# Kernel tuning notes

Measured on AMD Instinct MI355X. Metric: run time of the kernel, lower is better.

## Reference

```python
import jax, jax.numpy as jnp
import numpy as np

# Hard-coded dims from the module
D, L, R, H, M, T = 64, 90, 5760, 1024, 1024, 20
N_OUT = 3
B = 64  # per-timestep batch; feature has B*T rows


def setup_inputs() -> dict:
    key = jax.random.key(0)
    ks = jax.random.split(key, 20)
    def w(i, shape, fan_in):
        return jax.random.normal(ks[i], shape, dtype=jnp.float32) * (1.0 / np.sqrt(fan_in))
    return {
        "feature": jax.random.normal(ks[0], (B * T, L, D), dtype=jnp.float32),
        # additive attention params (alpha over L locations)
        "attn_Wx": w(1, (D, D), D),
        "attn_Wh": w(2, (H, D), H),
        "attn_v": w(3, (D,), D),
        # LSTM (PyTorch gate order i,f,g,o)
        "W_ih": w(4, (4 * H, R), R),
        "W_hh": w(5, (4 * H, H), H),
        "b_ih": jnp.zeros((4 * H,), jnp.float32),
        "b_hh": jnp.zeros((4 * H,), jnp.float32),
        # output head
        "Wh_w": w(6, (M, H), H),
        "Wh_b": jnp.zeros((M,), jnp.float32),
        "Wy_w": w(7, (M, R), R),
        "Wu_w": w(8, (N_OUT, M), M),
        "Wu_b": jnp.zeros((N_OUT,), jnp.float32),
        # LSTM-state initializers
        "iWh_w": w(9, (H, D), D),
        "iWh_b": jnp.zeros((H,), jnp.float32),
        "iWc_w": w(10, (H, D), D),
        "iWc_b": jnp.zeros((H,), jnp.float32),
    }


def reference(feature, attn_Wx, attn_Wh, attn_v, W_ih, W_hh, b_ih, b_hh,
              Wh_w, Wh_b, Wy_w, Wu_w, Wu_b, iWh_w, iWh_b, iWc_w, iWc_b):
    batch = feature.shape[0] // T
    seq = feature.reshape(batch, T, L, D).transpose(1, 0, 2, 3)  # [T,B,L,D]

    # initializeLSTM (no_grad in the original -> stop_gradient)
    f0 = jnp.mean(seq[0], axis=1)                                  # [B,D]
    h0 = jax.lax.stop_gradient(jnp.tanh(f0 @ iWh_w.T + iWh_b))     # [B,H]
    c0 = jax.lax.stop_gradient(jnp.tanh(f0 @ iWc_w.T + iWc_b))     # [B,H]

    def step(carry, xt):  # xt: [B,L,D]
        h, c = carry
        # additive attention over L locations
        e = jnp.tanh(jnp.einsum('bld,da->bla', xt, attn_Wx)
                     + (h @ attn_Wh)[:, None, :]) @ attn_v          # [B,L]
        alpha = jax.nn.softmax(e, axis=1)
        visual = (xt * alpha[:, :, None]).reshape(-1, R)            # [B,R]
        # single LSTM step (PyTorch gate order i,f,g,o)
        gates = visual @ W_ih.T + b_ih + h @ W_hh.T + b_hh          # [B,4H]
        i, f, g, o = jnp.split(gates, 4, axis=-1)
        c = jax.nn.sigmoid(f) * c + jax.nn.sigmoid(i) * jnp.tanh(g)
        h = jax.nn.sigmoid(o) * jnp.tanh(c)
        # ut = Wu(Wh(h) + Wy(visual)); dropout omitted for determinism
        ut = (h @ Wh_w.T + Wh_b + visual @ Wy_w.T) @ Wu_w.T + Wu_b  # [B,n_out]
        return (h, c), ut

    _, outs = jax.lax.scan(step, (h0, c0), seq)                     # [T,B,n_out]
    return outs.transpose(1, 0, 2).reshape(batch * T, -1)
```

## Files before the change

### kernel.cpp

```cpp
#include <hip/hip_runtime.h>
#include <math.h>

typedef _Float16 half8 __attribute__((ext_vector_type(8)));
typedef _Float16 half4v __attribute__((ext_vector_type(4)));
typedef _Float16 half2v __attribute__((ext_vector_type(2)));
typedef float floatx16 __attribute__((ext_vector_type(16)));

#define TT 20
#define NB 64
#define LL 90
#define DD 64
#define RR 5760
#define HH 1024
#define NG 4096
#define KT 6784
#define CH0 90
#define CHT 106

__device__ __forceinline__ float sigm(float x) { return 1.f / (1.f + expf(-x)); }

__global__ __launch_bounds__(256) void k_conv2(const float* __restrict__ s1, _Float16* __restrict__ d1, int n1,
                                               const float* __restrict__ s2, _Float16* __restrict__ d2, int n2) {
    int i = (blockIdx.x * 256 + threadIdx.x) * 4;
    const float* s; _Float16* d;
    if (i < n1) { s = s1 + i; d = d1 + i; }
    else if ((i -= n1) < n2) { s = s2 + i; d = d2 + i; }
    else return;
    const float4 v = *(const float4*)s;
    half4v o;
    o[0] = (_Float16)v.x; o[1] = (_Float16)v.y;
    o[2] = (_Float16)v.z; o[3] = (_Float16)v.w;
    *(half4v*)d = o;
}

__global__ __launch_bounds__(256) void k_whT(const float* __restrict__ Wh, _Float16* __restrict__ WhT) {
    const int idx = blockIdx.x * 256 + threadIdx.x;
    const int a = idx >> 8, k4 = (idx & 255) * 4;
    half4v o;
#pragma unroll
    for (int u = 0; u < 4; ++u) o[u] = (_Float16)Wh[(size_t)(k4 + u) * DD + a];
    *(half4v*)(WhT + (size_t)a * HH + k4) = o;
}

__global__ __launch_bounds__(256) void k_xproj(const float* __restrict__ feat,
                                               const float* __restrict__ Wx,
                                               _Float16* __restrict__ xp) {
    __shared__ float sWx[DD * DD];
    __shared__ float sx[16 * DD];
    const int row = blockIdx.x;
    const int tid = threadIdx.x;
    for (int e = tid * 4; e < DD * DD; e += 1024)
        *(float4*)(sWx + e) = *(const float4*)(Wx + e);
    const int a4 = tid & 15, lg = tid >> 4;
    const float* frow = feat + (size_t)row * RR;
    for (int lb = 0; lb < LL; lb += 16) {
        __syncthreads();
        { int e = tid * 4; int ls = e >> 6, dd = e & 63;
          if (lb + ls < LL) *(float4*)(sx + e) = *(const float4*)(frow + (lb + ls) * DD + dd); }
        __syncthreads();
        const int l = lb + lg;
        if (l < LL) {
            float a0 = 0, a1 = 0, a2 = 0, a3 = 0;
            for (int dd = 0; dd < DD; ++dd) {
                const float xv = sx[lg * DD + dd];
                const float4 wv = *(const float4*)(sWx + dd * DD + a4 * 4);
                a0 += xv * wv.x; a1 += xv * wv.y; a2 += xv * wv.z; a3 += xv * wv.w;
            }
            half4v o;
            o[0] = (_Float16)a0; o[1] = (_Float16)a1; o[2] = (_Float16)a2; o[3] = (_Float16)a3;
            *(half4v*)(xp + (size_t)row * RR + l * DD + a4 * 4) = o;
        }
    }
}

__global__ __launch_bounds__(256) void k_init(const float* __restrict__ feat,
        const float* __restrict__ iWh_w, const float* __restrict__ iWh_b,
        const float* __restrict__ iWc_w, const float* __restrict__ iWc_b,
        float* __restrict__ h, float* __restrict__ c, _Float16* __restrict__ h16) {
    __shared__ float f0p[4][DD];
    __shared__ float f0[DD];
    const int b = blockIdx.x, tid = threadIdx.x;
    const int dd = tid & 63, lg = tid >> 6;
    const float* frow = feat + (size_t)(b * TT) * RR;
    float p = 0;
    for (int l = lg; l < LL; l += 4) p += frow[l * DD + dd];
    f0p[lg][dd] = p;
    __syncthreads();
    if (tid < DD) f0[tid] = (f0p[0][tid] + f0p[1][tid] + f0p[2][tid] + f0p[3][tid]) * (1.0f / LL);
    __syncthreads();
    for (int o = tid; o < HH; o += 256) {
        float ah = iWh_b[o], ac = iWc_b[o];
        for (int d0 = 0; d0 < DD; d0 += 4) {
            const float4 wh = *(const float4*)(iWh_w + (size_t)o * DD + d0);
            const float4 wc = *(const float4*)(iWc_w + (size_t)o * DD + d0);
            ah += f0[d0] * wh.x + f0[d0 + 1] * wh.y + f0[d0 + 2] * wh.z + f0[d0 + 3] * wh.w;
            ac += f0[d0] * wc.x + f0[d0 + 1] * wc.y + f0[d0 + 2] * wc.z + f0[d0 + 3] * wc.w;
        }
        const float hv = tanhf(ah), cv = tanhf(ac);
        h[b * HH + o] = hv; c[b * HH + o] = cv;
        h16[b * HH + o] = (_Float16)hv;
    }
}

__global__ __launch_bounds__(512) void k_step(int tattn, int do_cell,
        const float* __restrict__ gpart, const float* __restrict__ b_ih,
        const float* __restrict__ b_hh, const float* __restrict__ cin,
        float* __restrict__ cout, _Float16* __restrict__ h16,
        _Float16* __restrict__ H16, const float* __restrict__ h0buf,
        const float* __restrict__ feat, const _Float16* __restrict__ xp,
        const _Float16* __restrict__ WhT, const float* __restrict__ v,
        _Float16* __restrict__ V16) {
    __shared__ float sh[HH];
    __shared__ float hWhp[8][DD];
    __shared__ float hWh[DD];
    __shared__ float sv[DD];
    __shared__ float ep[LL][4];
    __shared__ float se[128];
    __shared__ float red[128];
    __shared__ float salpha[LL];
    const int b = blockIdx.x, qv = blockIdx.y, tid = threadIdx.x;
    const int t = tattn;
    if (tid < DD) sv[tid] = v[tid];

    if (do_cell) {
        const int j0 = tid * 2;
        float ag[4][2];
#pragma unroll
        for (int g = 0; g < 4; ++g) { ag[g][0] = 0.f; ag[g][1] = 0.f; }
#pragma unroll
        for (int sp = 0; sp < 8; ++sp) {
            const float* P = gpart + ((size_t)sp * NB + b) * NG;
#pragma unroll
            for (int g = 0; g < 4; ++g) {
                const float2 pv = *(const float2*)(P + g * HH + j0);
                ag[g][0] += pv.x; ag[g][1] += pv.y;
            }
        }
#pragma unroll
        for (int g = 0; g < 4; ++g) {
            const float2 bi = *(const float2*)(b_ih + g * HH + j0);
            const float2 bh = *(const float2*)(b_hh + g * HH + j0);
            ag[g][0] += bi.x + bh.x; ag[g][1] += bi.y + bh.y;
        }
        const float2 cold = *(const float2*)(cin + (size_t)b * HH + j0);
        float co[2] = { cold.x, cold.y };
        float2 cnew; half2v hh2;
#pragma unroll
        for (int q = 0; q < 2; ++q) {
            const float cv = sigm(ag[1][q]) * co[q] + sigm(ag[0][q]) * tanhf(ag[2][q]);
            const float hv = sigm(ag[3][q]) * tanhf(cv);
            ((float*)&cnew)[q] = cv;
            hh2[q] = (_Float16)hv;
            sh[j0 + q] = hv;
        }
        *(float2*)(cout + (size_t)b * HH + j0) = cnew;
        *(half2v*)(h16 + (size_t)b * HH + j0) = hh2;
        *(half2v*)(H16 + ((size_t)(t - 1) * NB + b) * HH + j0) = hh2;
    } else {
        for (int e = tid; e < HH; e += 512) sh[e] = h0buf[(size_t)b * HH + e];
    }
    __syncthreads();
    if (t >= TT) return;

    { const int a = tid & 63, q8 = tid >> 6;
      const _Float16* Wq = WhT + (size_t)a * HH + q8 * 128;
      const float* shq = sh + q8 * 128;
      float p = 0.f;
#pragma unroll
      for (int k = 0; k < 128; k += 8) {
          const half8 wv = *(const half8*)(Wq + k);
#pragma unroll
          for (int u = 0; u < 8; ++u) p += shq[k + u] * (float)wv[u];
      }
      hWhp[q8][a] = p; }
    __syncthreads();
    if (tid < DD) {
        float s = 0.f;
#pragma unroll
        for (int q = 0; q < 8; ++q) s += hWhp[q][tid];
        hWh[tid] = s;
    }
    __syncthreads();

    const size_t frow = (size_t)(b * TT + t) * RR;
    if (tid < 360) {
        const int l = tid >> 2, qq = tid & 3;
        const _Float16* xr = xp + frow + l * DD + qq * 16;
        const half8 x0 = *(const half8*)(xr);
        const half8 x1 = *(const half8*)(xr + 8);
        float acc = 0.f;
#pragma unroll
        for (int i = 0; i < 8; ++i)
            acc += tanhf((float)x0[i] + hWh[qq * 16 + i]) * sv[qq * 16 + i];
#pragma unroll
        for (int i = 0; i < 8; ++i)
            acc += tanhf((float)x1[i] + hWh[qq * 16 + 8 + i]) * sv[qq * 16 + 8 + i];
        ep[l][qq] = acc;
    }
    __syncthreads();
    if (tid < LL) se[tid] = ep[tid][0] + ep[tid][1] + ep[tid][2] + ep[tid][3];
    else if (tid < 128) se[tid] = -1e30f;
    __syncthreads();
    if (tid < 128) red[tid] = se[tid];
    __syncthreads();
    for (int s = 64; s; s >>= 1) { if (tid < s) red[tid] = fmaxf(red[tid], red[tid + s]); __syncthreads(); }
    const float mx = red[0];
    __syncthreads();
    float ex = 0.f;
    if (tid < LL) { ex = expf(se[tid] - mx); salpha[tid] = ex; }
    if (tid < 128) red[tid] = ex;
    __syncthreads();
    for (int s = 64; s; s >>= 1) { if (tid < s) red[tid] += red[tid + s]; __syncthreads(); }
    const float inv = 1.f / red[0];
    __syncthreads();
    if (tid < LL) salpha[tid] *= inv;
    __syncthreads();

    _Float16* vout = V16 + ((size_t)t * NB + b) * RR;
    const float* fr = feat + frow;
    const int ebeg = qv * 1440;
    const int e = ebeg + tid * 4;
    if (e < ebeg + 1440) {
        const float4 u4 = *(const float4*)(fr + e);
        const float al = salpha[e >> 6];
        half4v o;
        o[0] = (_Float16)(u4.x * al); o[1] = (_Float16)(u4.y * al);
        o[2] = (_Float16)(u4.z * al); o[3] = (_Float16)(u4.w * al);
        *(half4v*)(vout + e) = o;
    }
}

__device__ __forceinline__ void stage_tile(const char* src, size_t stride, char* lds, int ln) {
    const char* g = src + (size_t)(ln >> 3) * stride + (((ln & 7) ^ (ln >> 3)) << 4);
#pragma unroll
    for (int i = 0; i < 8; ++i)
        __builtin_amdgcn_global_load_lds(
            (const __attribute__((address_space(1))) void*)(g + (size_t)(i * 8) * stride),
            (__attribute__((address_space(3))) void*)(lds + i * 1024), 16, 0, 0);
}

struct Src2 { const char* p0; size_t s0; const char* p1; size_t s1; };

__device__ __forceinline__ const char* chunk_ptr(const Src2& s, int c, size_t& stride) {
    if (c < CH0) { stride = s.s0; return s.p0 + (size_t)c * 128; }
    stride = s.s1; return s.p1 + (size_t)(c - CH0) * 128;
}

__global__ __launch_bounds__(128) void k_gates(int t, const _Float16* __restrict__ V16,
        const _Float16* __restrict__ h16, const _Float16* __restrict__ Wih,
        const _Float16* __restrict__ Whh, float* __restrict__ gpart) {
    __shared__ char smem[65536];
    const int bid = blockIdx.x;
    const int kb = bid >> 6;
    const int nt = ((bid & 7) << 3) | ((bid >> 3) & 7);
    const int tid = threadIdx.x, w = tid >> 6, ln = tid & 63;
    char* wlds = smem + w * 32768;

    const _Float16* Vt = V16 + (size_t)t * NB * RR;
    Src2 As = { (const char*)Vt, (size_t)RR * 2, (const char*)h16, (size_t)HH * 2 };
    Src2 Bs = { (const char*)(Wih + (size_t)(nt * 64) * RR), (size_t)RR * 2,
                (const char*)(Whh + (size_t)(nt * 64) * HH), (size_t)HH * 2 };

    floatx16 acc00, acc01, acc10, acc11;
#pragma unroll
    for (int i = 0; i < 16; ++i) { acc00[i] = 0.f; acc01[i] = 0.f; acc10[i] = 0.f; acc11[i] = 0.f; }

    const int start = kb * 2 + w;
    const int r = ln & 31;
    const int xsw = (r & 7) << 4;
    const int fo = (ln >> 5) * 16;
    const int rbyte = r * 128;

    int c = start, bsel = 0;
    { size_t st; const char* p = chunk_ptr(As, c, st); stage_tile(p, st, wlds, ln);
      p = chunk_ptr(Bs, c, st); stage_tile(p, st, wlds + 8192, ln); }
    while (true) {
        const int cn = c + 16;
        if (cn < CHT) {
            char* nl = wlds + ((bsel ^ 1) << 14);
            size_t st; const char* p = chunk_ptr(As, cn, st); stage_tile(p, st, nl, ln);
            p = chunk_ptr(Bs, cn, st); stage_tile(p, st, nl + 8192, ln);
            asm volatile("s_waitcnt vmcnt(16)" ::: "memory");
        } else {
            asm volatile("s_waitcnt vmcnt(0)" ::: "memory");
        }
        __builtin_amdgcn_sched_barrier(0);
        const char* LA = wlds + (bsel << 14);
        const char* LB = LA + 8192;
#pragma unroll
        for (int kk = 0; kk < 4; ++kk) {
            const int o = ((kk * 32 + fo) ^ xsw);
            const half8 a0 = *(const half8*)(LA + rbyte + o);
            const half8 a1 = *(const half8*)(LA + 4096 + rbyte + o);
            const half8 b0 = *(const half8*)(LB + rbyte + o);
            const half8 b1 = *(const half8*)(LB + 4096 + rbyte + o);
            acc00 = __builtin_amdgcn_mfma_f32_32x32x16_f16(a0, b0, acc00, 0, 0, 0);
            acc01 = __builtin_amdgcn_mfma_f32_32x32x16_f16(a0, b1, acc01, 0, 0, 0);
            acc10 = __builtin_amdgcn_mfma_f32_32x32x16_f16(a1, b0, acc10, 0, 0, 0);
            acc11 = __builtin_amdgcn_mfma_f32_32x32x16_f16(a1, b1, acc11, 0, 0, 0);
        }
        if (cn >= CHT) break;
        c = cn; bsel ^= 1;
    }
    __syncthreads();
    float* Rg = (float*)(smem + w * 16384);
    const int rbase = 4 * (ln >> 5), lr = ln & 31;
#pragma unroll
    for (int q = 0; q < 16; ++q) {
        const int row = rbase + (q & 3) + 8 * (q >> 2);
        Rg[row * 64 + lr]             = acc00[q];
        Rg[row * 64 + 32 + lr]        = acc01[q];
        Rg[(row + 32) * 64 + lr]      = acc10[q];
        Rg[(row + 32) * 64 + 32 + lr] = acc11[q];
    }
    __syncthreads();
    const float* R0 = (const float*)smem;
    const float* R1 = (const float*)(smem + 16384);
    float* Cout = gpart + (size_t)kb * (NB * NG);
    for (int e = tid * 4; e < 4096; e += 512) {
        const float4 u = *(const float4*)(R0 + e);
        const float4 v2 = *(const float4*)(R1 + e);
        float4 s2; s2.x = u.x + v2.x; s2.y = u.y + v2.y; s2.z = u.z + v2.z; s2.w = u.w + v2.w;
        const int row = e >> 6, col = e & 63;
        *(float4*)(Cout + (size_t)row * NG + nt * 64 + col) = s2;
    }
}

__global__ __launch_bounds__(256) void k_wfuse(const float* __restrict__ Wy,
        const float* __restrict__ Whw, const float* __restrict__ Wu,
        const float* __restrict__ Whb, const float* __restrict__ Wub,
        _Float16* __restrict__ Wyu16, float* __restrict__ cst) {
    __shared__ float sWu[3 * HH];
    __shared__ float part[4][3][64];
    const int tid = threadIdx.x;
    for (int e = tid * 4; e < 3 * HH; e += 1024)
        *(float4*)(sWu + e) = *(const float4*)(Wu + e);
    __syncthreads();
    if (blockIdx.x == CHT) {
        float a0 = 0, a1 = 0, a2 = 0;
        for (int m = tid; m < HH; m += 256) {
            const float wb = Whb[m];
            a0 += sWu[m] * wb; a1 += sWu[HH + m] * wb; a2 += sWu[2 * HH + m] * wb;
        }
        __shared__ float rp[3][256];
        rp[0][tid] = a0; rp[1][tid] = a1; rp[2][tid] = a2;
        __syncthreads();
        for (int s = 128; s; s >>= 1) {
            if (tid < s) { rp[0][tid] += rp[0][tid + s]; rp[1][tid] += rp[1][tid + s]; rp[2][tid] += rp[2][tid + s]; }
            __syncthreads();
        }
        if (tid < 3) cst[tid] = rp[tid][0] + Wub[tid];
        return;
    }
    const int kk = tid & 63, qm = tid >> 6;
    const int k = blockIdx.x * 64 + kk;
    const float* src; size_t ld;
    if (blockIdx.x < CH0) { src = Wy + k; ld = RR; }
    else { src = Whw + (k - RR); ld = HH; }
    float a0 = 0, a1 = 0, a2 = 0;
    for (int m = qm * 256; m < qm * 256 + 256; ++m) {
        const float val = src[(size_t)m * ld];
        a0 += sWu[m] * val; a1 += sWu[HH + m] * val; a2 += sWu[2 * HH + m] * val;
    }
    part[qm][0][kk] = a0; part[qm][1][kk] = a1; part[qm][2][kk] = a2;
    __syncthreads();
    if (tid < 192) {
        const int j = tid >> 6, k2 = tid & 63;
        const float s = part[0][j][k2] + part[1][j][k2] + part[2][j][k2] + part[3][j][k2];
        Wyu16[(size_t)j * KT + blockIdx.x * 64 + k2] = (_Float16)s;
    }
}

__global__ __launch_bounds__(256) void k_final2(const _Float16* __restrict__ V16,
        const _Float16* __restrict__ H16, const _Float16* __restrict__ Wyu,
        const float* __restrict__ cst, float* __restrict__ out) {
    __shared__ float rp[4][3];
    const int r = blockIdx.x, tid = threadIdx.x;
    const _Float16* vrow = V16 + (size_t)r * RR;
    const _Float16* hrow = H16 + (size_t)r * HH;
    float a0 = 0, a1 = 0, a2 = 0;
    for (int e = tid * 8; e < KT; e += 2048) {
        half8 x;
        if (e < RR) x = *(const half8*)(vrow + e);
        else        x = *(const half8*)(hrow + (e - RR));
        const half8 w0 = *(const half8*)(Wyu + e);
        const half8 w1 = *(const half8*)(Wyu + KT + e);
        const half8 w2 = *(const half8*)(Wyu + 2 * KT + e);
#pragma unroll
        for (int i = 0; i < 8; ++i) {
            const float xv = (float)x[i];
            a0 += xv * (float)w0[i]; a1 += xv * (float)w1[i]; a2 += xv * (float)w2[i];
        }
    }
    for (int o = 32; o > 0; o >>= 1) {
        a0 += __shfl_down(a0, o, 64); a1 += __shfl_down(a1, o, 64); a2 += __shfl_down(a2, o, 64);
    }
    const int wv = tid >> 6;
    if ((tid & 63) == 0) { rp[wv][0] = a0; rp[wv][1] = a1; rp[wv][2] = a2; }
    __syncthreads();
    if (tid < 3) {
        const float x = rp[0][tid] + rp[1][tid] + rp[2][tid] + rp[3][tid] + cst[tid];
        const int b = r & 63, ts = r >> 6;
        out[((size_t)b * TT + ts) * 3 + tid] = x;
    }
}

extern "C" void kernel_launch(void* const* d_in, const int* in_sizes, int n_in,
                              void* d_out, int out_size, void* d_ws, size_t ws_size,
                              hipStream_t stream) {
    (void)in_sizes; (void)n_in; (void)out_size;
    const float* feature = (const float*)d_in[0];
    const float* attn_Wx = (const float*)d_in[1];
    const float* attn_Wh = (const float*)d_in[2];
    const float* attn_v  = (const float*)d_in[3];
    const float* W_ih    = (const float*)d_in[4];
    const float* W_hh    = (const float*)d_in[5];
    const float* b_ih    = (const float*)d_in[6];
    const float* b_hh    = (const float*)d_in[7];
    const float* Wh_w    = (const float*)d_in[8];
    const float* Wh_b    = (const float*)d_in[9];
    const float* Wy_w    = (const float*)d_in[10];
    const float* Wu_w    = (const float*)d_in[11];
    const float* Wu_b    = (const float*)d_in[12];
    const float* iWh_w   = (const float*)d_in[13];
    const float* iWh_b   = (const float*)d_in[14];
    const float* iWc_w   = (const float*)d_in[15];
    const float* iWc_b   = (const float*)d_in[16];
    float* out = (float*)d_out;

    char* ws = (char*)d_ws;
    size_t off = 0;
    auto alloc = [&](size_t bytes) { void* p = ws + off; off += (bytes + 255) & ~(size_t)255; return p; };
    _Float16* Wih16 = (_Float16*)alloc((size_t)NG * RR * 2);
    _Float16* Whh16 = (_Float16*)alloc((size_t)NG * HH * 2);
    _Float16* WhT16 = (_Float16*)alloc((size_t)DD * HH * 2);
    _Float16* xp16  = (_Float16*)alloc((size_t)1280 * RR * 2);
    _Float16* V16   = (_Float16*)alloc((size_t)TT * NB * RR * 2);
    _Float16* H16   = (_Float16*)alloc((size_t)TT * NB * HH * 2);
    float*    hbuf  = (float*)alloc((size_t)NB * HH * 4);
    float*    cb0   = (float*)alloc((size_t)NB * HH * 4);
    float*    cb1   = (float*)alloc((size_t)NB * HH * 4);
    _Float16* h16   = (_Float16*)alloc((size_t)NB * HH * 2);
    float*    gpart = (float*)alloc((size_t)8 * NB * NG * 4);
    _Float16* Wyu16 = (_Float16*)alloc((size_t)3 * KT * 2);
    float*    cstb  = (float*)alloc(16);
    if (ws_size < off) return;

    const int nconv = NG * RR + NG * HH;
    k_conv2<<<(nconv / 4 + 255) / 256, 256, 0, stream>>>(W_ih, Wih16, NG * RR,
                                                         W_hh, Whh16, NG * HH);
    k_whT<<<64, 256, 0, stream>>>(attn_Wh, WhT16);
    k_xproj<<<1280, 256, 0, stream>>>(feature, attn_Wx, xp16);
    k_wfuse<<<CHT + 1, 256, 0, stream>>>(Wy_w, Wh_w, Wu_w, Wh_b, Wu_b, Wyu16, cstb);
    k_init<<<64, 256, 0, stream>>>(feature, iWh_w, iWh_b, iWc_w, iWc_b, hbuf, cb0, h16);

    k_step<<<dim3(64, 4), 512, 0, stream>>>(0, 0, gpart, b_ih, b_hh, cb0, cb1,
                                            h16, H16, hbuf, feature, xp16, WhT16,
                                            attn_v, V16);
    for (int t = 0; t < TT; ++t) {
        k_gates<<<512, 128, 0, stream>>>(t, V16, h16, Wih16, Whh16, gpart);
        const float* cin = (t & 1) ? cb1 : cb0;
        float* cou       = (t & 1) ? cb0 : cb1;
        k_step<<<dim3(64, 4), 512, 0, stream>>>(t + 1, 1, gpart, b_ih, b_hh, cin, cou,
                                                h16, H16, hbuf, feature, xp16, WhT16,
                                                attn_v, V16);
    }

    k_final2<<<1280, 256, 0, stream>>>(V16, H16, Wyu16, cstb, out);
}
```

Measured before the change: 649.5 us.

## Fuse attention/cell step and gate GEMM into one producer-consumer kernel

Merges the per-timestep attention/LSTM-cell kernel and the gate GEMM into a single launch. 64 producer blocks compute the cell update, attention and context vector, then signal a per-timestep atomic counter. The 448 consumer blocks first stage their weight tile, then spin on that counter before loading the activation tile. Split-K drops from 8 to 7 and a separate kernel finishes the last cell update. This roughly halves the kernel launches and overlaps weight loading with the producers' work. In exchange, each batch row now uses one 128-thread producer block instead of four 512-thread blocks, and correctness relies on the producers being resident while consumers spin.

Measured after the change: 1.438 ms. +121.4%, slower.

```diff
diff --git a/kernel.cpp b/kernel.cpp
--- a/kernel.cpp
+++ b/kernel.cpp
@@ -3,7 +3,6 @@
 
 typedef _Float16 half8 __attribute__((ext_vector_type(8)));
 typedef _Float16 half4v __attribute__((ext_vector_type(4)));
-typedef _Float16 half2v __attribute__((ext_vector_type(2)));
 typedef float floatx16 __attribute__((ext_vector_type(16)));
 
 #define TT 20
@@ -16,6 +15,10 @@
 #define KT 6784
 #define CH0 90
 #define CHT 106
+#define NPROD 64
+#define SPLITK 7
+#define NCONS 448
+#define KSTRIDE 14
 
 __device__ __forceinline__ float sigm(float x) { return 1.f / (1.f + expf(-x)); }
 
@@ -76,10 +79,12 @@
 __global__ __launch_bounds__(256) void k_init(const float* __restrict__ feat,
         const float* __restrict__ iWh_w, const float* __restrict__ iWh_b,
         const float* __restrict__ iWc_w, const float* __restrict__ iWc_b,
-        float* __restrict__ h, float* __restrict__ c, _Float16* __restrict__ h16) {
+        float* __restrict__ h, float* __restrict__ c, _Float16* __restrict__ h16,
+        int* __restrict__ done) {
     __shared__ float f0p[4][DD];
     __shared__ float f0[DD];
     const int b = blockIdx.x, tid = threadIdx.x;
+    if (b == 0 && tid < 32) done[tid] = 0;
     const int dd = tid & 63, lg = tid >> 6;
     const float* frow = feat + (size_t)(b * TT) * RR;
     float p = 0;
@@ -102,134 +107,6 @@
     }
 }
 
-__global__ __launch_bounds__(512) void k_step(int tattn, int do_cell,
-        const float* __restrict__ gpart, const float* __restrict__ b_ih,
-        const float* __restrict__ b_hh, const float* __restrict__ cin,
-        float* __restrict__ cout, _Float16* __restrict__ h16,
-        _Float16* __restrict__ H16, const float* __restrict__ h0buf,
-        const float* __restrict__ feat, const _Float16* __restrict__ xp,
-        const _Float16* __restrict__ WhT, const float* __restrict__ v,
-        _Float16* __restrict__ V16) {
-    __shared__ float sh[HH];
-    __shared__ float hWhp[8][DD];
-    __shared__ float hWh[DD];
-    __shared__ float sv[DD];
-    __shared__ float ep[LL][4];
-    __shared__ float se[128];
-    __shared__ float red[128];
-    __shared__ float salpha[LL];
-    const int b = blockIdx.x, qv = blockIdx.y, tid = threadIdx.x;
-    const int t = tattn;
-    if (tid < DD) sv[tid] = v[tid];
-
-    if (do_cell) {
-        const int j0 = tid * 2;
-        float ag[4][2];
-#pragma unroll
-        for (int g = 0; g < 4; ++g) { ag[g][0] = 0.f; ag[g][1] = 0.f; }
-#pragma unroll
-        for (int sp = 0; sp < 8; ++sp) {
-            const float* P = gpart + ((size_t)sp * NB + b) * NG;
-#pragma unroll
-            for (int g = 0; g < 4; ++g) {
-                const float2 pv = *(const float2*)(P + g * HH + j0);
-                ag[g][0] += pv.x; ag[g][1] += pv.y;
-            }
-        }
-#pragma unroll
-        for (int g = 0; g < 4; ++g) {
-            const float2 bi = *(const float2*)(b_ih + g * HH + j0);
-            const float2 bh = *(const float2*)(b_hh + g * HH + j0);
-            ag[g][0] += bi.x + bh.x; ag[g][1] += bi.y + bh.y;
-        }
-        const float2 cold = *(const float2*)(cin + (size_t)b * HH + j0);
-        float co[2] = { cold.x, cold.y };
-        float2 cnew; half2v hh2;
-#pragma unroll
-        for (int q = 0; q < 2; ++q) {
-            const float cv = sigm(ag[1][q]) * co[q] + sigm(ag[0][q]) * tanhf(ag[2][q]);
-            const float hv = sigm(ag[3][q]) * tanhf(cv);
-            ((float*)&cnew)[q] = cv;
-            hh2[q] = (_Float16)hv;
-            sh[j0 + q] = hv;
-        }
-        *(float2*)(cout + (size_t)b * HH + j0) = cnew;
-        *(half2v*)(h16 + (size_t)b * HH + j0) = hh2;
-        *(half2v*)(H16 + ((size_t)(t - 1) * NB + b) * HH + j0) = hh2;
-    } else {
-        for (int e = tid; e < HH; e += 512) sh[e] = h0buf[(size_t)b * HH + e];
-    }
-    __syncthreads();
-    if (t >= TT) return;
-
-    { const int a = tid & 63, q8 = tid >> 6;
-      const _Float16* Wq = WhT + (size_t)a * HH + q8 * 128;
-      const float* shq = sh + q8 * 128;
-      float p = 0.f;
-#pragma unroll
-      for (int k = 0; k < 128; k += 8) {
-          const half8 wv = *(const half8*)(Wq + k);
-#pragma unroll
-          for (int u = 0; u < 8; ++u) p += shq[k + u] * (float)wv[u];
-      }
-      hWhp[q8][a] = p; }
-    __syncthreads();
-    if (tid < DD) {
-        float s = 0.f;
-#pragma unroll
-        for (int q = 0; q < 8; ++q) s += hWhp[q][tid];
-        hWh[tid] = s;
-    }
-    __syncthreads();
-
-    const size_t frow = (size_t)(b * TT + t) * RR;
-    if (tid < 360) {
-        const int l = tid >> 2, qq = tid & 3;
-        const _Float16* xr = xp + frow + l * DD + qq * 16;
-        const half8 x0 = *(const half8*)(xr);
-        const half8 x1 = *(const half8*)(xr + 8);
-        float acc = 0.f;
-#pragma unroll
-        for (int i = 0; i < 8; ++i)
-            acc += tanhf((float)x0[i] + hWh[qq * 16 + i]) * sv[qq * 16 + i];
-#pragma unroll
-        for (int i = 0; i < 8; ++i)
-            acc += tanhf((float)x1[i] + hWh[qq * 16 + 8 + i]) * sv[qq * 16 + 8 + i];
-        ep[l][qq] = acc;
-    }
-    __syncthreads();
-    if (tid < LL) se[tid] = ep[tid][0] + ep[tid][1] + ep[tid][2] + ep[tid][3];
-    else if (tid < 128) se[tid] = -1e30f;
-    __syncthreads();
-    if (tid < 128) red[tid] = se[tid];
-    __syncthreads();
-    for (int s = 64; s; s >>= 1) { if (tid < s) red[tid] = fmaxf(red[tid], red[tid + s]); __syncthreads(); }
-    const float mx = red[0];
-    __syncthreads();
-    float ex = 0.f;
-    if (tid < LL) { ex = expf(se[tid] - mx); salpha[tid] = ex; }
-    if (tid < 128) red[tid] = ex;
-    __syncthreads();
-    for (int s = 64; s; s >>= 1) { if (tid < s) red[tid] += red[tid + s]; __syncthreads(); }
-    const float inv = 1.f / red[0];
-    __syncthreads();
-    if (tid < LL) salpha[tid] *= inv;
-    __syncthreads();
-
-    _Float16* vout = V16 + ((size_t)t * NB + b) * RR;
-    const float* fr = feat + frow;
-    const int ebeg = qv * 1440;
-    const int e = ebeg + tid * 4;
-    if (e < ebeg + 1440) {
-        const float4 u4 = *(const float4*)(fr + e);
-        const float al = salpha[e >> 6];
-        half4v o;
-        o[0] = (_Float16)(u4.x * al); o[1] = (_Float16)(u4.y * al);
-        o[2] = (_Float16)(u4.z * al); o[3] = (_Float16)(u4.w * al);
-        *(half4v*)(vout + e) = o;
-    }
-}
-
 __device__ __forceinline__ void stage_tile(const char* src, size_t stride, char* lds, int ln) {
     const char* g = src + (size_t)(ln >> 3) * stride + (((ln & 7) ^ (ln >> 3)) << 4);
 #pragma unroll
@@ -246,14 +123,136 @@
     stride = s.s1; return s.p1 + (size_t)(c - CH0) * 128;
 }
 
-__global__ __launch_bounds__(128) void k_gates(int t, const _Float16* __restrict__ V16,
-        const _Float16* __restrict__ h16, const _Float16* __restrict__ Wih,
-        const _Float16* __restrict__ Whh, float* __restrict__ gpart) {
+__global__ __launch_bounds__(128) void k_sf(int t,
+        const _Float16* __restrict__ Wih, const _Float16* __restrict__ Whh,
+        const _Float16* __restrict__ WhT, const float* __restrict__ v,
+        const float* __restrict__ b_ih, const float* __restrict__ b_hh,
+        const float* __restrict__ hbuf, const float* __restrict__ cin,
+        float* __restrict__ cout, _Float16* __restrict__ h16,
+        _Float16* __restrict__ H16, const float* __restrict__ feat,
+        const _Float16* __restrict__ xp, _Float16* __restrict__ V16,
+        float* __restrict__ gpart, int* __restrict__ done) {
     __shared__ char smem[65536];
-    const int bid = blockIdx.x;
-    const int kb = bid >> 6;
-    const int nt = ((bid & 7) << 3) | ((bid >> 3) & 7);
-    const int tid = threadIdx.x, w = tid >> 6, ln = tid & 63;
+    const int bid = blockIdx.x, tid = threadIdx.x;
+
+    if (bid < NPROD) {
+        const int b = bid;
+        float* sh     = (float*)smem;
+        float* hWhp   = sh + HH;
+        float* hWh    = hWhp + 128;
+        float* sv     = hWh + 64;
+        float* salpha = sv + 64;
+        float* red2   = salpha + 96;
+        if (tid < DD) sv[tid] = v[tid];
+
+        if (t > 0) {
+            const int j0 = tid * 8;
+            float ag[4][8];
+#pragma unroll
+            for (int g = 0; g < 4; ++g)
+#pragma unroll
+                for (int u = 0; u < 8; ++u) ag[g][u] = 0.f;
+            for (int sp = 0; sp < SPLITK; ++sp) {
+                const float* P = gpart + ((size_t)sp * NB + b) * NG;
+#pragma unroll
+                for (int g = 0; g < 4; ++g) {
+                    const float4 p0 = *(const float4*)(P + g * HH + j0);
+                    const float4 p1 = *(const float4*)(P + g * HH + j0 + 4);
+                    ag[g][0] += p0.x; ag[g][1] += p0.y; ag[g][2] += p0.z; ag[g][3] += p0.w;
+                    ag[g][4] += p1.x; ag[g][5] += p1.y; ag[g][6] += p1.z; ag[g][7] += p1.w;
+                }
+            }
+#pragma unroll
+            for (int g = 0; g < 4; ++g) {
+                const float* bi = b_ih + g * HH + j0;
+                const float* bh = b_hh + g * HH + j0;
+#pragma unroll
+                for (int u = 0; u < 8; ++u) ag[g][u] += bi[u] + bh[u];
+            }
+            const float4 ca = *(const float4*)(cin + (size_t)b * HH + j0);
+            const float4 cb4 = *(const float4*)(cin + (size_t)b * HH + j0 + 4);
+            const float co[8] = { ca.x, ca.y, ca.z, ca.w, cb4.x, cb4.y, cb4.z, cb4.w };
+            float cn[8]; half8 h8;
+#pragma unroll
+            for (int u = 0; u < 8; ++u) {
+                const float cv = sigm(ag[1][u]) * co[u] + sigm(ag[0][u]) * tanhf(ag[2][u]);
+                const float hv = sigm(ag[3][u]) * tanhf(cv);
+                cn[u] = cv; h8[u] = (_Float16)hv; sh[j0 + u] = hv;
+            }
+            *(float4*)(cout + (size_t)b * HH + j0)     = make_float4(cn[0], cn[1], cn[2], cn[3]);
+            *(float4*)(cout + (size_t)b * HH + j0 + 4) = make_float4(cn[4], cn[5], cn[6], cn[7]);
+            *(half8*)(h16 + (size_t)b * HH + j0) = h8;
+            *(half8*)(H16 + ((size_t)(t - 1) * NB + b) * HH + j0) = h8;
+        } else {
+            for (int e = tid; e < HH; e += 128) sh[e] = hbuf[(size_t)b * HH + e];
+        }
+        __syncthreads();
+
+        { const int a = tid & 63, hf = tid >> 6;
+          const _Float16* Wq = WhT + (size_t)a * HH + hf * 512;
+          const float* shq = sh + hf * 512;
+          float p = 0.f;
+#pragma unroll
+          for (int k = 0; k < 512; k += 8) {
+              const half8 wv = *(const half8*)(Wq + k);
+#pragma unroll
+              for (int u = 0; u < 8; ++u) p += shq[k + u] * (float)wv[u];
+          }
+          hWhp[hf * 64 + a] = p; }
+        __syncthreads();
+        if (tid < DD) hWh[tid] = hWhp[tid] + hWhp[64 + tid];
+        __syncthreads();
+
+        float ev = -1e30f;
+        if (tid < LL) {
+            const _Float16* xr = xp + ((size_t)b * TT + t) * RR + tid * DD;
+            float acc = 0.f;
+#pragma unroll
+            for (int i8 = 0; i8 < 8; ++i8) {
+                const half8 x = *(const half8*)(xr + i8 * 8);
+#pragma unroll
+                for (int u = 0; u < 8; ++u)
+                    acc += tanhf((float)x[u] + hWh[i8 * 8 + u]) * sv[i8 * 8 + u];
+            }
+            ev = acc;
+        }
+        float m = ev;
+        for (int o = 32; o; o >>= 1) m = fmaxf(m, __shfl_down(m, o, 64));
+        if ((tid & 63) == 0) red2[tid >> 6] = m;
+        __syncthreads();
+        const float mx = fmaxf(red2[0], red2[1]);
+        __syncthreads();
+        const float ex = (tid < LL) ? expf(ev - mx) : 0.f;
+        float s = ex;
+        for (int o = 32; o; o >>= 1) s += __shfl_down(s, o, 64);
+        if ((tid & 63) == 0) red2[tid >> 6] = s;
+        __syncthreads();
+        const float inv = 1.f / (red2[0] + red2[1]);
+        if (tid < LL) salpha[tid] = ex * inv;
+        __syncthreads();
+
+        _Float16* vout = V16 + ((size_t)t * NB + b) * RR;
+        const float* fr = feat + ((size_t)b * TT + t) * RR;
+        for (int e = tid * 4; e < RR; e += 512) {
+            const float4 u4 = *(const float4*)(fr + e);
+            const float al = salpha[e >> 6];
+            half4v o;
+            o[0] = (_Float16)(u4.x * al); o[1] = (_Float16)(u4.y * al);
+            o[2] = (_Float16)(u4.z * al); o[3] = (_Float16)(u4.w * al);
+            *(half4v*)(vout + e) = o;
+        }
+        __threadfence();
+        __syncthreads();
+        if (tid == 0)
+            __hip_atomic_fetch_add(done + t, 1, __ATOMIC_RELEASE, __HIP_MEMORY_SCOPE_AGENT);
+        return;
+    }
+
+    const int cb = bid - NPROD;
+    const int a8 = cb & 7, q = cb >> 3;
+    const int kb = q % 7, hi = q / 7;
+    const int nt = (a8 << 3) | hi;
+    const int w = tid >> 6, ln = tid & 63;
     char* wlds = smem + w * 32768;
 
     const _Float16* Vt = V16 + (size_t)t * NB * RR;
@@ -272,10 +271,14 @@
     const int rbyte = r * 128;
 
     int c = start, bsel = 0;
-    { size_t st; const char* p = chunk_ptr(As, c, st); stage_tile(p, st, wlds, ln);
-      p = chunk_ptr(Bs, c, st); stage_tile(p, st, wlds + 8192, ln); }
+    { size_t st; const char* p = chunk_ptr(Bs, c, st); stage_tile(p, st, wlds + 8192, ln); }
+    while (__hip_atomic_load(done + t, __ATOMIC_RELAXED, __HIP_MEMORY_SCOPE_AGENT) < NPROD)
+        __builtin_amdgcn_s_sleep(32);
+    __threadfence();
+    { size_t st; const char* p = chunk_ptr(As, c, st); stage_tile(p, st, wlds, ln); }
+
     while (true) {
-        const int cn = c + 16;
+        const int cn = c + KSTRIDE;
         if (cn < CHT) {
             char* nl = wlds + ((bsel ^ 1) << 14);
             size_t st; const char* p = chunk_ptr(As, cn, st); stage_tile(p, st, nl, ln);
@@ -306,12 +309,12 @@
     float* Rg = (float*)(smem + w * 16384);
     const int rbase = 4 * (ln >> 5), lr = ln & 31;
 #pragma unroll
-    for (int q = 0; q < 16; ++q) {
-        const int row = rbase + (q & 3) + 8 * (q >> 2);
-        Rg[row * 64 + lr]             = acc00[q];
-        Rg[row * 64 + 32 + lr]        = acc01[q];
-        Rg[(row + 32) * 64 + lr]      = acc10[q];
-        Rg[(row + 32) * 64 + 32 + lr] = acc11[q];
+    for (int qq = 0; qq < 16; ++qq) {
+        const int row = rbase + (qq & 3) + 8 * (qq >> 2);
+        Rg[row * 64 + lr]             = acc00[qq];
+        Rg[row * 64 + 32 + lr]        = acc01[qq];
+        Rg[(row + 32) * 64 + lr]      = acc10[qq];
+        Rg[(row + 32) * 64 + 32 + lr] = acc11[qq];
     }
     __syncthreads();
     const float* R0 = (const float*)smem;
@@ -324,6 +327,45 @@
         const int row = e >> 6, col = e & 63;
         *(float4*)(Cout + (size_t)row * NG + nt * 64 + col) = s2;
     }
+}
+
+__global__ __launch_bounds__(128) void k_cell_last(const float* __restrict__ gpart,
+        const float* __restrict__ b_ih, const float* __restrict__ b_hh,
+        const float* __restrict__ cin, _Float16* __restrict__ H16) {
+    const int b = blockIdx.x, tid = threadIdx.x;
+    const int j0 = tid * 8;
+    float ag[4][8];
+#pragma unroll
+    for (int g = 0; g < 4; ++g)
+#pragma unroll
+        for (int u = 0; u < 8; ++u) ag[g][u] = 0.f;
+    for (int sp = 0; sp < SPLITK; ++sp) {
+        const float* P = gpart + ((size_t)sp * NB + b) * NG;
+#pragma unroll
+        for (int g = 0; g < 4; ++g) {
+            const float4 p0 = *(const float4*)(P + g * HH + j0);
+            const float4 p1 = *(const float4*)(P + g * HH + j0 + 4);
+            ag[g][0] += p0.x; ag[g][1] += p0.y; ag[g][2] += p0.z; ag[g][3] += p0.w;
+            ag[g][4] += p1.x; ag[g][5] += p1.y; ag[g][6] += p1.z; ag[g][7] += p1.w;
+        }
+    }
+#pragma unroll
+    for (int g = 0; g < 4; ++g) {
+        const float* bi = b_ih + g * HH + j0;
+        const float* bh = b_hh + g * HH + j0;
+#pragma unroll
+        for (int u = 0; u < 8; ++u) ag[g][u] += bi[u] + bh[u];
+    }
+    const float4 ca = *(const float4*)(cin + (size_t)b * HH + j0);
+    const float4 cb4 = *(const float4*)(cin + (size_t)b * HH + j0 + 4);
+    const float co[8] = { ca.x, ca.y, ca.z, ca.w, cb4.x, cb4.y, cb4.z, cb4.w };
+    half8 h8;
+#pragma unroll
+    for (int u = 0; u < 8; ++u) {
+        const float cv = sigm(ag[1][u]) * co[u] + sigm(ag[0][u]) * tanhf(ag[2][u]);
+        h8[u] = (_Float16)(sigm(ag[3][u]) * tanhf(cv));
+    }
+    *(half8*)(H16 + ((size_t)19 * NB + b) * HH + j0) = h8;
 }
 
 __global__ __launch_bounds__(256) void k_wfuse(const float* __restrict__ Wy,
@@ -441,9 +483,10 @@
     float*    cb0   = (float*)alloc((size_t)NB * HH * 4);
     float*    cb1   = (float*)alloc((size_t)NB * HH * 4);
     _Float16* h16   = (_Float16*)alloc((size_t)NB * HH * 2);
-    float*    gpart = (float*)alloc((size_t)8 * NB * NG * 4);
+    float*    gpart = (float*)alloc((size_t)SPLITK * NB * NG * 4);
     _Float16* Wyu16 = (_Float16*)alloc((size_t)3 * KT * 2);
     float*    cstb  = (float*)alloc(16);
+    int*      done  = (int*)alloc(128);
     if (ws_size < off) return;
 
     const int nconv = NG * RR + NG * HH;
@@ -452,19 +495,16 @@
     k_whT<<<64, 256, 0, stream>>>(attn_Wh, WhT16);
     k_xproj<<<1280, 256, 0, stream>>>(feature, attn_Wx, xp16);
     k_wfuse<<<CHT + 1, 256, 0, stream>>>(Wy_w, Wh_w, Wu_w, Wh_b, Wu_b, Wyu16, cstb);
-    k_init<<<64, 256, 0, stream>>>(feature, iWh_w, iWh_b, iWc_w, iWc_b, hbuf, cb0, h16);
-
-    k_step<<<dim3(64, 4), 512, 0, stream>>>(0, 0, gpart, b_ih, b_hh, cb0, cb1,
-                                            h16, H16, hbuf, feature, xp16, WhT16,
-                                            attn_v, V16);
+    k_init<<<64, 256, 0, stream>>>(feature, iWh_w, iWh_b, iWc_w, iWc_b, hbuf, cb1, h16, done);
+
     for (int t = 0; t < TT; ++t) {
-        k_gates<<<512, 128, 0, stream>>>(t, V16, h16, Wih16, Whh16, gpart);
         const float* cin = (t & 1) ? cb1 : cb0;
         float* cou       = (t & 1) ? cb0 : cb1;
-        k_step<<<dim3(64, 4), 512, 0, stream>>>(t + 1, 1, gpart, b_ih, b_hh, cin, cou,
-                                                h16, H16, hbuf, feature, xp16, WhT16,
-                                                attn_v, V16);
-    }
+        k_sf<<<NPROD + NCONS, 128, 0, stream>>>(t, Wih16, Whh16, WhT16, attn_v,
+                                                b_ih, b_hh, hbuf, cin, cou, h16, H16,
+                                                feature, xp16, V16, gpart, done);
+    }
+    k_cell_last<<<64, 128, 0, stream>>>(gpart, b_ih, b_hh, cb0, H16);
 
     k_final2<<<1280, 256, 0, stream>>>(V16, H16, Wyu16, cstb, out);
 }
```

## Fuse output-head dot products into step kernel and merge prep kernels

Applied to the files above, without the earlier changes.

Moves the per-row output projection (visual and h against the fused Wyu weights) into the per-step kernel, so it produces 3-wide partial sums instead of storing full V16/H16 histories for a final pass. The old k_final2 becomes a tiny combine kernel, and the V16 buffer shrinks to a single timestep. The step kernel drops from a 64x4 grid to 64 blocks, each looping over the whole visual row, which reduces parallelism on the serial critical path. The WhT transpose is also folded into the weight conversion kernel to save a launch.

After: 687.3 us. 5.8% more time.

```diff
diff --git a/kernel.cpp b/kernel.cpp
--- a/kernel.cpp
+++ b/kernel.cpp
@@ -16,12 +16,24 @@
 #define KT 6784
 #define CH0 90
 #define CHT 106
+#define SPLITK 8
 
 __device__ __forceinline__ float sigm(float x) { return 1.f / (1.f + expf(-x)); }
 
-__global__ __launch_bounds__(256) void k_conv2(const float* __restrict__ s1, _Float16* __restrict__ d1, int n1,
-                                               const float* __restrict__ s2, _Float16* __restrict__ d2, int n2) {
-    int i = (blockIdx.x * 256 + threadIdx.x) * 4;
+__global__ __launch_bounds__(256) void k_prep(const float* __restrict__ s1, _Float16* __restrict__ d1, int n1,
+                                              const float* __restrict__ s2, _Float16* __restrict__ d2, int n2,
+                                              int ncb, const float* __restrict__ Wh, _Float16* __restrict__ WhT) {
+    const int bid = blockIdx.x, tid = threadIdx.x;
+    if (bid >= ncb) {
+        const int idx = (bid - ncb) * 256 + tid;
+        const int a = idx >> 8, k4 = (idx & 255) * 4;
+        half4v o;
+#pragma unroll
+        for (int u = 0; u < 4; ++u) o[u] = (_Float16)Wh[(size_t)(k4 + u) * DD + a];
+        *(half4v*)(WhT + (size_t)a * HH + k4) = o;
+        return;
+    }
+    int i = (bid * 256 + tid) * 4;
     const float* s; _Float16* d;
     if (i < n1) { s = s1 + i; d = d1 + i; }
     else if ((i -= n1) < n2) { s = s2 + i; d = d2 + i; }
@@ -31,15 +43,6 @@
     o[0] = (_Float16)v.x; o[1] = (_Float16)v.y;
     o[2] = (_Float16)v.z; o[3] = (_Float16)v.w;
     *(half4v*)d = o;
-}
-
-__global__ __launch_bounds__(256) void k_whT(const float* __restrict__ Wh, _Float16* __restrict__ WhT) {
-    const int idx = blockIdx.x * 256 + threadIdx.x;
-    const int a = idx >> 8, k4 = (idx & 255) * 4;
-    half4v o;
-#pragma unroll
-    for (int u = 0; u < 4; ++u) o[u] = (_Float16)Wh[(size_t)(k4 + u) * DD + a];
-    *(half4v*)(WhT + (size_t)a * HH + k4) = o;
 }
 
 __global__ __launch_bounds__(256) void k_xproj(const float* __restrict__ feat,
@@ -102,14 +105,15 @@
     }
 }
 
-__global__ __launch_bounds__(512) void k_step(int tattn, int do_cell,
+__global__ __launch_bounds__(512) void k_step(int t, int do_cell,
         const float* __restrict__ gpart, const float* __restrict__ b_ih,
         const float* __restrict__ b_hh, const float* __restrict__ cin,
         float* __restrict__ cout, _Float16* __restrict__ h16,
-        _Float16* __restrict__ H16, const float* __restrict__ h0buf,
-        const float* __restrict__ feat, const _Float16* __restrict__ xp,
-        const _Float16* __restrict__ WhT, const float* __restrict__ v,
-        _Float16* __restrict__ V16) {
+        const float* __restrict__ h0buf, const float* __restrict__ feat,
+        const _Float16* __restrict__ xp, const _Float16* __restrict__ WhT,
+        const float* __restrict__ v, _Float16* __restrict__ V16,
+        const _Float16* __restrict__ Wyu, float* __restrict__ vpart,
+        float* __restrict__ hpart) {
     __shared__ float sh[HH];
     __shared__ float hWhp[8][DD];
     __shared__ float hWh[DD];
@@ -118,9 +122,11 @@
     __shared__ float se[128];
     __shared__ float red[128];
     __shared__ float salpha[LL];
-    const int b = blockIdx.x, qv = blockIdx.y, tid = threadIdx.x;
-    const int t = tattn;
+    __shared__ float hdr[8][6];
+    const int b = blockIdx.x, tid = threadIdx.x;
     if (tid < DD) sv[tid] = v[tid];
+    float hp0 = 0.f, hp1 = 0.f, hp2 = 0.f;
+    float vp0 = 0.f, vp1 = 0.f, vp2 = 0.f;
 
     if (do_cell) {
         const int j0 = tid * 2;
@@ -128,7 +134,7 @@
 #pragma unroll
         for (int g = 0; g < 4; ++g) { ag[g][0] = 0.f; ag[g][1] = 0.f; }
 #pragma unroll
-        for (int sp = 0; sp < 8; ++sp) {
+        for (int sp = 0; sp < SPLITK; ++sp) {
             const float* P = gpart + ((size_t)sp * NB + b) * NG;
 #pragma unroll
             for (int g = 0; g < 4; ++g) {
@@ -155,78 +161,106 @@
         }
         *(float2*)(cout + (size_t)b * HH + j0) = cnew;
         *(half2v*)(h16 + (size_t)b * HH + j0) = hh2;
-        *(half2v*)(H16 + ((size_t)(t - 1) * NB + b) * HH + j0) = hh2;
+        const float h0f = (float)hh2[0], h1f = (float)hh2[1];
+        hp0 = h0f * (float)Wyu[0 * KT + RR + j0] + h1f * (float)Wyu[0 * KT + RR + j0 + 1];
+        hp1 = h0f * (float)Wyu[1 * KT + RR + j0] + h1f * (float)Wyu[1 * KT + RR + j0 + 1];
+        hp2 = h0f * (float)Wyu[2 * KT + RR + j0] + h1f * (float)Wyu[2 * KT + RR + j0 + 1];
     } else {
         for (int e = tid; e < HH; e += 512) sh[e] = h0buf[(size_t)b * HH + e];
     }
     __syncthreads();
-    if (t >= TT) return;
-
-    { const int a = tid & 63, q8 = tid >> 6;
-      const _Float16* Wq = WhT + (size_t)a * HH + q8 * 128;
-      const float* shq = sh + q8 * 128;
-      float p = 0.f;
-#pragma unroll
-      for (int k = 0; k < 128; k += 8) {
-          const half8 wv = *(const half8*)(Wq + k);
-#pragma unroll
-          for (int u = 0; u < 8; ++u) p += shq[k + u] * (float)wv[u];
-      }
-      hWhp[q8][a] = p; }
-    __syncthreads();
-    if (tid < DD) {
+
+    if (t < TT) {
+        { const int a = tid & 63, q8 = tid >> 6;
+          const _Float16* Wq = WhT + (size_t)a * HH + q8 * 128;
+          const float* shq = sh + q8 * 128;
+          float p = 0.f;
+#pragma unroll
+          for (int k = 0; k < 128; k += 8) {
+              const half8 wv = *(const half8*)(Wq + k);
+#pragma unroll
+              for (int u = 0; u < 8; ++u) p += shq[k + u] * (float)wv[u];
+          }
+          hWhp[q8][a] = p; }
+        __syncthreads();
+        if (tid < DD) {
+            float s = 0.f;
+#pragma unroll
+            for (int q = 0; q < 8; ++q) s += hWhp[q][tid];
+            hWh[tid] = s;
+        }
+        __syncthreads();
+
+        const size_t frow = (size_t)(b * TT + t) * RR;
+        if (tid < 360) {
+            const int l = tid >> 2, qq = tid & 3;
+            const _Float16* xr = xp + frow + l * DD + qq * 16;
+            const half8 x0 = *(const half8*)(xr);
+            const half8 x1 = *(const half8*)(xr + 8);
+            float acc = 0.f;
+#pragma unroll
+            for (int i = 0; i < 8; ++i)
+                acc += tanhf((float)x0[i] + hWh[qq * 16 + i]) * sv[qq * 16 + i];
+#pragma unroll
+            for (int i = 0; i < 8; ++i)
+                acc += tanhf((float)x1[i] + hWh[qq * 16 + 8 + i]) * sv[qq * 16 + 8 + i];
+            ep[l][qq] = acc;
+        }
+        __syncthreads();
+        if (tid < LL) se[tid] = ep[tid][0] + ep[tid][1] + ep[tid][2] + ep[tid][3];
+        else if (tid < 128) se[tid] = -1e30f;
+        __syncthreads();
+        if (tid < 128) red[tid] = se[tid];
+        __syncthreads();
+        for (int s = 64; s; s >>= 1) { if (tid < s) red[tid] = fmaxf(red[tid], red[tid + s]); __syncthreads(); }
+        const float mx = red[0];
+        __syncthreads();
+        float ex = 0.f;
+        if (tid < LL) { ex = expf(se[tid] - mx); salpha[tid] = ex; }
+        if (tid < 128) red[tid] = ex;
+        __syncthreads();
+        for (int s = 64; s; s >>= 1) { if (tid < s) red[tid] += red[tid + s]; __syncthreads(); }
+        const float inv = 1.f / red[0];
+        __syncthreads();
+        if (tid < LL) salpha[tid] *= inv;
+        __syncthreads();
+
+        _Float16* vout = V16 + (size_t)b * RR;
+        const float* fr = feat + frow;
+        for (int e = tid * 4; e < RR; e += 2048) {
+            const float4 u4 = *(const float4*)(fr + e);
+            const float al = salpha[e >> 6];
+            half4v o;
+            o[0] = (_Float16)(u4.x * al); o[1] = (_Float16)(u4.y * al);
+            o[2] = (_Float16)(u4.z * al); o[3] = (_Float16)(u4.w * al);
+            *(half4v*)(vout + e) = o;
+            const half4v w0 = *(const half4v*)(Wyu + e);
+            const half4v w1 = *(const half4v*)(Wyu + KT + e);
+            const half4v w2 = *(const half4v*)(Wyu + 2 * KT + e);
+#pragma unroll
+            for (int u = 0; u < 4; ++u) {
+                const float xv = (float)o[u];
+                vp0 += xv * (float)w0[u]; vp1 += xv * (float)w1[u]; vp2 += xv * (float)w2[u];
+            }
+        }
+    }
+
+    for (int o = 32; o; o >>= 1) {
+        hp0 += __shfl_down(hp0, o, 64); hp1 += __shfl_down(hp1, o, 64); hp2 += __shfl_down(hp2, o, 64);
+        vp0 += __shfl_down(vp0, o, 64); vp1 += __shfl_down(vp1, o, 64); vp2 += __shfl_down(vp2, o, 64);
+    }
+    if ((tid & 63) == 0) {
+        const int w = tid >> 6;
+        hdr[w][0] = hp0; hdr[w][1] = hp1; hdr[w][2] = hp2;
+        hdr[w][3] = vp0; hdr[w][4] = vp1; hdr[w][5] = vp2;
+    }
+    __syncthreads();
+    if (tid < 6) {
         float s = 0.f;
 #pragma unroll
-        for (int q = 0; q < 8; ++q) s += hWhp[q][tid];
-        hWh[tid] = s;
-    }
-    __syncthreads();
-
-    const size_t frow = (size_t)(b * TT + t) * RR;
-    if (tid < 360) {
-        const int l = tid >> 2, qq = tid & 3;
-        const _Float16* xr = xp + frow + l * DD + qq * 16;
-        const half8 x0 = *(const half8*)(xr);
-        const half8 x1 = *(const half8*)(xr + 8);
-        float acc = 0.f;
-#pragma unroll
-        for (int i = 0; i < 8; ++i)
-            acc += tanhf((float)x0[i] + hWh[qq * 16 + i]) * sv[qq * 16 + i];
-#pragma unroll
-        for (int i = 0; i < 8; ++i)
-            acc += tanhf((float)x1[i] + hWh[qq * 16 + 8 + i]) * sv[qq * 16 + 8 + i];
-        ep[l][qq] = acc;
-    }
-    __syncthreads();
-    if (tid < LL) se[tid] = ep[tid][0] + ep[tid][1] + ep[tid][2] + ep[tid][3];
-    else if (tid < 128) se[tid] = -1e30f;
-    __syncthreads();
-    if (tid < 128) red[tid] = se[tid];
-    __syncthreads();
-    for (int s = 64; s; s >>= 1) { if (tid < s) red[tid] = fmaxf(red[tid], red[tid + s]); __syncthreads(); }
-    const float mx = red[0];
-    __syncthreads();
-    float ex = 0.f;
-    if (tid < LL) { ex = expf(se[tid] - mx); salpha[tid] = ex; }
-    if (tid < 128) red[tid] = ex;
-    __syncthreads();
-    for (int s = 64; s; s >>= 1) { if (tid < s) red[tid] += red[tid + s]; __syncthreads(); }
-    const float inv = 1.f / red[0];
-    __syncthreads();
-    if (tid < LL) salpha[tid] *= inv;
-    __syncthreads();
-
-    _Float16* vout = V16 + ((size_t)t * NB + b) * RR;
-    const float* fr = feat + frow;
-    const int ebeg = qv * 1440;
-    const int e = ebeg + tid * 4;
-    if (e < ebeg + 1440) {
-        const float4 u4 = *(const float4*)(fr + e);
-        const float al = salpha[e >> 6];
-        half4v o;
-        o[0] = (_Float16)(u4.x * al); o[1] = (_Float16)(u4.y * al);
-        o[2] = (_Float16)(u4.z * al); o[3] = (_Float16)(u4.w * al);
-        *(half4v*)(vout + e) = o;
+        for (int w = 0; w < 8; ++w) s += hdr[w][tid];
+        if (tid < 3) { if (do_cell) hpart[((size_t)(t - 1) * NB + b) * 3 + tid] = s; }
+        else         { if (t < TT)  vpart[((size_t)t * NB + b) * 3 + (tid - 3)] = s; }
     }
 }
 
@@ -246,7 +280,7 @@
     stride = s.s1; return s.p1 + (size_t)(c - CH0) * 128;
 }
 
-__global__ __launch_bounds__(128) void k_gates(int t, const _Float16* __restrict__ V16,
+__global__ __launch_bounds__(128) void k_gates(const _Float16* __restrict__ V16,
         const _Float16* __restrict__ h16, const _Float16* __restrict__ Wih,
         const _Float16* __restrict__ Whh, float* __restrict__ gpart) {
     __shared__ char smem[65536];
@@ -256,8 +290,7 @@
     const int tid = threadIdx.x, w = tid >> 6, ln = tid & 63;
     char* wlds = smem + w * 32768;
 
-    const _Float16* Vt = V16 + (size_t)t * NB * RR;
-    Src2 As = { (const char*)Vt, (size_t)RR * 2, (const char*)h16, (size_t)HH * 2 };
+    Src2 As = { (const char*)V16, (size_t)RR * 2, (const char*)h16, (size_t)HH * 2 };
     Src2 Bs = { (const char*)(Wih + (size_t)(nt * 64) * RR), (size_t)RR * 2,
                 (const char*)(Whh + (size_t)(nt * 64) * HH), (size_t)HH * 2 };
 
@@ -371,38 +404,14 @@
     }
 }
 
-__global__ __launch_bounds__(256) void k_final2(const _Float16* __restrict__ V16,
-        const _Float16* __restrict__ H16, const _Float16* __restrict__ Wyu,
-        const float* __restrict__ cst, float* __restrict__ out) {
-    __shared__ float rp[4][3];
-    const int r = blockIdx.x, tid = threadIdx.x;
-    const _Float16* vrow = V16 + (size_t)r * RR;
-    const _Float16* hrow = H16 + (size_t)r * HH;
-    float a0 = 0, a1 = 0, a2 = 0;
-    for (int e = tid * 8; e < KT; e += 2048) {
-        half8 x;
-        if (e < RR) x = *(const half8*)(vrow + e);
-        else        x = *(const half8*)(hrow + (e - RR));
-        const half8 w0 = *(const half8*)(Wyu + e);
-        const half8 w1 = *(const half8*)(Wyu + KT + e);
-        const half8 w2 = *(const half8*)(Wyu + 2 * KT + e);
-#pragma unroll
-        for (int i = 0; i < 8; ++i) {
-            const float xv = (float)x[i];
-            a0 += xv * (float)w0[i]; a1 += xv * (float)w1[i]; a2 += xv * (float)w2[i];
-        }
-    }
-    for (int o = 32; o > 0; o >>= 1) {
-        a0 += __shfl_down(a0, o, 64); a1 += __shfl_down(a1, o, 64); a2 += __shfl_down(a2, o, 64);
-    }
-    const int wv = tid >> 6;
-    if ((tid & 63) == 0) { rp[wv][0] = a0; rp[wv][1] = a1; rp[wv][2] = a2; }
-    __syncthreads();
-    if (tid < 3) {
-        const float x = rp[0][tid] + rp[1][tid] + rp[2][tid] + rp[3][tid] + cst[tid];
-        const int b = r & 63, ts = r >> 6;
-        out[((size_t)b * TT + ts) * 3 + tid] = x;
-    }
+__global__ __launch_bounds__(256) void k_fin(const float* __restrict__ vpart,
+        const float* __restrict__ hpart, const float* __restrict__ cst,
+        float* __restrict__ out) {
+    const int idx = blockIdx.x * 256 + threadIdx.x;
+    if (idx >= TT * NB * 3) return;
+    const int r = idx / 3, j = idx - r * 3;
+    const int ts = r >> 6, b = r & 63;
+    out[((size_t)b * TT + ts) * 3 + j] = vpart[idx] + hpart[idx] + cst[j];
 }
 
 extern "C" void kernel_launch(void* const* d_in, const int* in_sizes, int n_in,
@@ -435,36 +444,37 @@
     _Float16* Whh16 = (_Float16*)alloc((size_t)NG * HH * 2);
     _Float16* WhT16 = (_Float16*)alloc((size_t)DD * HH * 2);
     _Float16* xp16  = (_Float16*)alloc((size_t)1280 * RR * 2);
-    _Float16* V16   = (_Float16*)alloc((size_t)TT * NB * RR * 2);
-    _Float16* H16   = (_Float16*)alloc((size_t)TT * NB * HH * 2);
+    _Float16* V16   = (_Float16*)alloc((size_t)NB * RR * 2);
     float*    hbuf  = (float*)alloc((size_t)NB * HH * 4);
     float*    cb0   = (float*)alloc((size_t)NB * HH * 4);
     float*    cb1   = (float*)alloc((size_t)NB * HH * 4);
     _Float16* h16   = (_Float16*)alloc((size_t)NB * HH * 2);
-    float*    gpart = (float*)alloc((size_t)8 * NB * NG * 4);
+    float*    gpart = (float*)alloc((size_t)SPLITK * NB * NG * 4);
     _Float16* Wyu16 = (_Float16*)alloc((size_t)3 * KT * 2);
+    float*    vpart = (float*)alloc((size_t)TT * NB * 3 * 4);
+    float*    hpart = (float*)alloc((size_t)TT * NB * 3 * 4);
     float*    cstb  = (float*)alloc(16);
     if (ws_size < off) return;
 
     const int nconv = NG * RR + NG * HH;
-    k_conv2<<<(nconv / 4 + 255) / 256, 256, 0, stream>>>(W_ih, Wih16, NG * RR,
-                                                         W_hh, Whh16, NG * HH);
-    k_whT<<<64, 256, 0, stream>>>(attn_Wh, WhT16);
+    const int ncb = (nconv / 4 + 255) / 256;
+    k_prep<<<ncb + 64, 256, 0, stream>>>(W_ih, Wih16, NG * RR, W_hh, Whh16, NG * HH,
+                                         ncb, attn_Wh, WhT16);
     k_xproj<<<1280, 256, 0, stream>>>(feature, attn_Wx, xp16);
     k_wfuse<<<CHT + 1, 256, 0, stream>>>(Wy_w, Wh_w, Wu_w, Wh_b, Wu_b, Wyu16, cstb);
     k_init<<<64, 256, 0, stream>>>(feature, iWh_w, iWh_b, iWc_w, iWc_b, hbuf, cb0, h16);
 
-    k_step<<<dim3(64, 4), 512, 0, stream>>>(0, 0, gpart, b_ih, b_hh, cb0, cb1,
-                                            h16, H16, hbuf, feature, xp16, WhT16,
-                                            attn_v, V16);
+    k_step<<<64, 512, 0, stream>>>(0, 0, gpart, b_ih, b_hh, cb0, cb1, h16, hbuf,
+                                   feature, xp16, WhT16, attn_v, V16, Wyu16,
+                                   vpart, hpart);
     for (int t = 0; t < TT; ++t) {
-        k_gates<<<512, 128, 0, stream>>>(t, V16, h16, Wih16, Whh16, gpart);
+        k_gates<<<512, 128, 0, stream>>>(V16, h16, Wih16, Whh16, gpart);
         const float* cin = (t & 1) ? cb1 : cb0;
         float* cou       = (t & 1) ? cb0 : cb1;
-        k_step<<<dim3(64, 4), 512, 0, stream>>>(t + 1, 1, gpart, b_ih, b_hh, cin, cou,
-                                                h16, H16, hbuf, feature, xp16, WhT16,
-                                                attn_v, V16);
-    }
-
-    k_final2<<<1280, 256, 0, stream>>>(V16, H16, Wyu16, cstb, out);
-}
+        k_step<<<64, 512, 0, stream>>>(t + 1, 1, gpart, b_ih, b_hh, cin, cou, h16, hbuf,
+                                       feature, xp16, WhT16, attn_v, V16, Wyu16,
+                                       vpart, hpart);
+    }
+
+    k_fin<<<15, 256, 0, stream>>>(vpart, hpart, cstb, out);
+}
```
